# Optimization experiments

Measured on AMD Instinct MI355X. Metric: run time of the kernel, lower is better.

## Reference

```python
import jax, jax.numpy as jnp
import numpy as np

EPS = 1e-4
NEG_BIAS = 0.01


def setup_inputs() -> dict:
    key = jax.random.key(0)
    ks = jax.random.split(key, 9)
    B, L, D_MODEL, HALF = 4, 4096, 2048, 32
    return {
        "u": jax.random.normal(ks[0], (B, L, D_MODEL), dtype=jnp.float32),
        "Lambda_unconstrained_re": jax.random.normal(ks[1], (HALF,), dtype=jnp.float32) * 0.1 - 1.0,
        "Lambda_im": jax.random.normal(ks[2], (HALF,), dtype=jnp.float32) * 3.0,
        "B_re": jax.random.normal(ks[3], (HALF, D_MODEL), dtype=jnp.float32) * 0.02,
        "B_im": jax.random.normal(ks[4], (HALF, D_MODEL), dtype=jnp.float32) * 0.02,
        "C_re": jax.random.normal(ks[5], (D_MODEL, HALF), dtype=jnp.float32) * 0.05,
        "C_im": jax.random.normal(ks[6], (D_MODEL, HALF), dtype=jnp.float32) * 0.05,
        "D": jax.random.normal(ks[7], (D_MODEL,), dtype=jnp.float32) * 0.1,
        "log_Delta": jax.random.uniform(ks[8], (2 * HALF,), minval=-3.0, maxval=-1.0, dtype=jnp.float32),
    }


def reference(u, Lambda_unconstrained_re, Lambda_im, B_re, B_im, C_re, C_im, D, log_Delta):
    half = Lambda_im.shape[0]
    # Constrained continuous-time eigenvalues: Re < 0 via softplus (inverse of init formula)
    lam_re = -(jax.nn.softplus(Lambda_unconstrained_re) + EPS + NEG_BIAS)
    Lam = lam_re + 1j * Lambda_im                      # [half]
    Delta = jnp.exp(log_Delta[:half])                  # per-state timestep
    # ZOH discretization
    Lam_bar = jnp.exp(Lam * Delta)                     # [half]
    B_tilde = (B_re + 1j * B_im).astype(jnp.complex64) # [half, d]
    B_bar = ((Lam_bar - 1.0) / Lam)[:, None] * B_tilde # [half, d]
    # Input projection: Bu[b,l,n]
    Bu = jnp.einsum("bld,nd->bln", u.astype(jnp.complex64), B_bar)
    a = jnp.broadcast_to(Lam_bar, Bu.shape)

    def op(e1, e2):
        a1, b1 = e1
        a2, b2 = e2
        return (a1 * a2, a2 * b1 + b2)

    # Parallel associative scan of x_t = Lam_bar * x_{t-1} + Bu_t along time axis
    _, xs = jax.lax.associative_scan(op, (a, Bu), axis=1)  # [b, l, half]
    C_tilde = (C_re + 1j * C_im).astype(jnp.complex64)     # [d, half]
    # Conjugate symmetry -> 2 * real part, plus skip connection D * u
    y = 2.0 * jnp.real(jnp.einsum("bln,dn->bld", xs, C_tilde)) + D * u
    return y
```

## Files before the change

kernel.cpp:

```cpp
#include <hip/hip_runtime.h>
#include <math.h>

#define M_ROWS 16384
#define DM     2048
#define NJ     64
#define L_SEQ  4096

typedef __bf16 bf16x8 __attribute__((ext_vector_type(8)));
typedef float  f32x4  __attribute__((ext_vector_type(4)));

constexpr size_t OB_BBART = 0;
constexpr size_t OB_CCT   = 256 * 1024;
constexpr size_t OB_BUT   = 512 * 1024;
constexpr size_t OB_XST   = 512 * 1024 + 4194304;

static __device__ __forceinline__ unsigned short f2bf(float f) {
  unsigned int u = __float_as_uint(f);
  u = (u + 0x7fffu + ((u >> 16) & 1u)) >> 16;
  return (unsigned short)u;
}

__global__ void k_prep(const float* __restrict__ lam_ur, const float* __restrict__ lam_im,
                       const float* __restrict__ log_dt,
                       const float* __restrict__ Bre, const float* __restrict__ Bim,
                       const float* __restrict__ Cre, const float* __restrict__ Cim,
                       unsigned short* __restrict__ bbarT, unsigned short* __restrict__ ccT) {
  const int idx = blockIdx.x * 256 + threadIdx.x;
  {
    const int j = idx >> 11, d = idx & 2047, n = j >> 1;
    float x = lam_ur[n];
    float sp = (x > 20.f) ? x : log1pf(expf(x));
    float lre = -(sp + 1.0e-4f + 0.01f);
    float lim = lam_im[n];
    float dt = expf(log_dt[n]);
    float er = expf(lre * dt);
    float Are = er * cosf(lim * dt);
    float Aim = er * sinf(lim * dt);
    float den = lre * lre + lim * lim;
    float cre = ((Are - 1.f) * lre + Aim * lim) / den;
    float cim = (Aim * lre - (Are - 1.f) * lim) / den;
    float br = Bre[n * DM + d], bi = Bim[n * DM + d];
    float v = (j & 1) ? (cre * bi + cim * br) : (cre * br - cim * bi);
    bbarT[(size_t)j * DM + d] = f2bf(v);
  }
  {
    const int j = idx & 63, d = idx >> 6, n = j >> 1;
    float v = (j & 1) ? (-2.f * Cim[d * 32 + n]) : (2.f * Cre[d * 32 + n]);
    ccT[(size_t)d * NJ + j] = f2bf(v);
  }
}

__global__ __launch_bounds__(256) void k_bu(const float* __restrict__ u,
                                            const unsigned short* __restrict__ bbarT,
                                            float* __restrict__ bu_t) {
  __shared__ __align__(16) unsigned short As[16][72];
  const int t = threadIdx.x;
  const int wave = t >> 6, lane = t & 63;
  const int m0 = blockIdx.x * 16;
  const int l15 = lane & 15, kq8 = (lane >> 4) * 8;
  const int srow = t >> 4, scol = (t & 15) * 4;
  const float* up = u + (size_t)(m0 + srow) * DM + scol;
  const unsigned short* bp = bbarT + (size_t)(wave * 16 + l15) * DM + kq8;
  f32x4 acc = {0.f, 0.f, 0.f, 0.f};
  for (int k0 = 0; k0 < DM; k0 += 64) {
    float4 v = *(const float4*)(up + k0);
    __syncthreads();
    ushort4 w4;
    w4.x = f2bf(v.x); w4.y = f2bf(v.y); w4.z = f2bf(v.z); w4.w = f2bf(v.w);
    *(ushort4*)&As[srow][scol] = w4;
    __syncthreads();
    bf16x8 a0 = *(const bf16x8*)&As[l15][kq8];
    bf16x8 a1 = *(const bf16x8*)&As[l15][32 + kq8];
    bf16x8 b0 = *(const bf16x8*)(bp + k0);
    bf16x8 b1 = *(const bf16x8*)(bp + k0 + 32);
    acc = __builtin_amdgcn_mfma_f32_16x16x32_bf16(a0, b0, acc, 0, 0, 0);
    acc = __builtin_amdgcn_mfma_f32_16x16x32_bf16(a1, b1, acc, 0, 0, 0);
  }
  const int j = wave * 16 + l15;
  const int orow = m0 + (lane >> 4) * 4;
  *(f32x4*)&bu_t[(size_t)j * M_ROWS + orow] = acc;
}

__global__ __launch_bounds__(256) void k_scan(const float* __restrict__ bu_t,
                                              const float* __restrict__ lam_ur,
                                              const float* __restrict__ lam_im,
                                              const float* __restrict__ log_dt,
                                              unsigned short* __restrict__ xs_t) {
  __shared__ float sre[L_SEQ + 256], sim[L_SEQ + 256];
  __shared__ float2 P[256];
  const int n = blockIdx.x;
  const int b = blockIdx.y;
  const int t = threadIdx.x;
  float x = lam_ur[n];
  float sp = (x > 20.f) ? x : log1pf(expf(x));
  float lre = -(sp + 1.0e-4f + 0.01f);
  float lim = lam_im[n];
  float dt = expf(log_dt[n]);
  float er = expf(lre * dt);
  const float Are = er * cosf(lim * dt);
  const float Aim = er * sinf(lim * dt);
  const float* pr = bu_t + (size_t)(2 * n) * M_ROWS + (size_t)b * L_SEQ;
  const float* pi = bu_t + (size_t)(2 * n + 1) * M_ROWS + (size_t)b * L_SEQ;
#pragma unroll
  for (int i0 = 4 * t; i0 < L_SEQ; i0 += 1024) {
    float4 vr = *(const float4*)(pr + i0);
    float4 vi = *(const float4*)(pi + i0);
    const float rr[4] = {vr.x, vr.y, vr.z, vr.w};
    const float ii[4] = {vi.x, vi.y, vi.z, vi.w};
#pragma unroll
    for (int q = 0; q < 4; ++q) {
      int e = i0 + q, ee = e + (e >> 4);
      sre[ee] = rr[q];
      sim[ee] = ii[q];
    }
  }
  __syncthreads();
  float lre16[16], lim16[16];
  float xre = 0.f, xim = 0.f;
#pragma unroll
  for (int i = 0; i < 16; ++i) {
    float bre = sre[17 * t + i], bim = sim[17 * t + i];
    float nr = Are * xre - Aim * xim + bre;
    float ni = Are * xim + Aim * xre + bim;
    xre = nr; xim = ni;
    lre16[i] = nr; lim16[i] = ni;
  }
  float Mre = Are, Mim = Aim;
#pragma unroll
  for (int k = 0; k < 4; ++k) {
    float nr = Mre * Mre - Mim * Mim;
    float ni = 2.f * Mre * Mim;
    Mre = nr; Mim = ni;
  }
  float pre = xre, pim = xim;
  P[t] = make_float2(pre, pim);
  __syncthreads();
  float msre = Mre, msim = Mim;
  for (int s = 1; s < 256; s <<= 1) {
    float2 prev = (t >= s) ? P[t - s] : make_float2(0.f, 0.f);
    __syncthreads();
    pre += msre * prev.x - msim * prev.y;
    pim += msre * prev.y + msim * prev.x;
    P[t] = make_float2(pre, pim);
    float nr = msre * msre - msim * msim;
    float ni = 2.f * msre * msim;
    msre = nr; msim = ni;
    __syncthreads();
  }
  float2 E = (t == 0) ? make_float2(0.f, 0.f) : P[t - 1];
  float pwre = Are, pwim = Aim;
#pragma unroll
  for (int i = 0; i < 16; ++i) {
    sre[17 * t + i] = lre16[i] + pwre * E.x - pwim * E.y;
    sim[17 * t + i] = lim16[i] + pwre * E.y + pwim * E.x;
    float nr = pwre * Are - pwim * Aim;
    float ni = pwre * Aim + pwim * Are;
    pwre = nr; pwim = ni;
  }
  __syncthreads();
  unsigned int* xr = (unsigned int*)(xs_t + (size_t)(2 * n) * M_ROWS + (size_t)b * L_SEQ);
  unsigned int* xi = (unsigned int*)(xs_t + (size_t)(2 * n + 1) * M_ROWS + (size_t)b * L_SEQ);
  for (int i = t; i < L_SEQ / 2; i += 256) {
    int e0 = 2 * i, e1 = 2 * i + 1;
    int p0 = e0 + (e0 >> 4), p1 = e1 + (e1 >> 4);
    xr[i] = ((unsigned int)f2bf(sre[p1]) << 16) | f2bf(sre[p0]);
    xi[i] = ((unsigned int)f2bf(sim[p1]) << 16) | f2bf(sim[p0]);
  }
}

__global__ __launch_bounds__(256) void k_out(const unsigned short* __restrict__ xs_t,
                                             const unsigned short* __restrict__ ccT,
                                             const float* __restrict__ u,
                                             const float* __restrict__ Dv,
                                             float* __restrict__ y) {
  __shared__ __align__(16) char smem[64 * 132 * 4];
  unsigned short (*As)[72] = (unsigned short(*)[72])smem;
  float (*Es)[132] = (float(*)[132])smem;
  const int t = threadIdx.x;
  const int wave = t >> 6, lane = t & 63;
  const int m0 = blockIdx.x * 64;
  const int d0 = blockIdx.y * 128;
  const int l15 = lane & 15, kq8 = (lane >> 4) * 8;
#pragma unroll
  for (int p = 0; p < 8; ++p) {
    int idx = t + 256 * p;
    int j = idx >> 5, r2 = idx & 31;
    unsigned int v = *(const unsigned int*)(xs_t + (size_t)j * M_ROWS + m0 + 2 * r2);
    As[2 * r2][j] = (unsigned short)(v & 0xffffu);
    As[2 * r2 + 1][j] = (unsigned short)(v >> 16);
  }
  __syncthreads();
  bf16x8 a0 = *(const bf16x8*)&As[wave * 16 + l15][kq8];
  bf16x8 a1 = *(const bf16x8*)&As[wave * 16 + l15][32 + kq8];
  f32x4 acc[8];
#pragma unroll
  for (int c = 0; c < 8; ++c) acc[c] = (f32x4){0.f, 0.f, 0.f, 0.f};
#pragma unroll
  for (int c = 0; c < 8; ++c) {
    const unsigned short* cp = ccT + (size_t)(d0 + c * 16 + l15) * NJ + kq8;
    bf16x8 b0 = *(const bf16x8*)cp;
    bf16x8 b1 = *(const bf16x8*)(cp + 32);
    acc[c] = __builtin_amdgcn_mfma_f32_16x16x32_bf16(a0, b0, acc[c], 0, 0, 0);
    acc[c] = __builtin_amdgcn_mfma_f32_16x16x32_bf16(a1, b1, acc[c], 0, 0, 0);
  }
  __syncthreads();
#pragma unroll
  for (int c = 0; c < 8; ++c)
#pragma unroll
    for (int i = 0; i < 4; ++i)
      Es[wave * 16 + (lane >> 4) * 4 + i][c * 16 + l15] = acc[c][i];
  __syncthreads();
#pragma unroll
  for (int p = 0; p < 8; ++p) {
    int idx = t + 256 * p;
    int row = idx >> 5;
    int c4 = (idx & 31) * 4;
    f32x4 e = *(const f32x4*)&Es[row][c4];
    const size_t off = (size_t)(m0 + row) * DM + d0 + c4;
    float4 uu = *(const float4*)&u[off];
    float4 dd = *(const float4*)&Dv[d0 + c4];
    float4 o;
    o.x = e[0] + dd.x * uu.x;
    o.y = e[1] + dd.y * uu.y;
    o.z = e[2] + dd.z * uu.z;
    o.w = e[3] + dd.w * uu.w;
    *(float4*)&y[off] = o;
  }
}

extern "C" void kernel_launch(void* const* d_in, const int* in_sizes, int n_in,
                              void* d_out, int out_size, void* d_ws, size_t ws_size,
                              hipStream_t stream) {
  const float* u      = (const float*)d_in[0];
  const float* lam_ur = (const float*)d_in[1];
  const float* lam_im = (const float*)d_in[2];
  const float* B_re   = (const float*)d_in[3];
  const float* B_im   = (const float*)d_in[4];
  const float* C_re   = (const float*)d_in[5];
  const float* C_im   = (const float*)d_in[6];
  const float* Dv     = (const float*)d_in[7];
  const float* log_dt = (const float*)d_in[8];
  float* y = (float*)d_out;
  char* ws = (char*)d_ws;

  unsigned short* bbarT = (unsigned short*)(ws + OB_BBART);
  unsigned short* ccT   = (unsigned short*)(ws + OB_CCT);
  float*          bu_t  = (float*)(ws + OB_BUT);
  unsigned short* xs_t  = (unsigned short*)(ws + OB_XST);

  k_prep<<<512, 256, 0, stream>>>(lam_ur, lam_im, log_dt, B_re, B_im, C_re, C_im, bbarT, ccT);
  k_bu<<<M_ROWS / 16, 256, 0, stream>>>(u, bbarT, bu_t);
  k_scan<<<dim3(32, 4), 256, 0, stream>>>(bu_t, lam_ur, lam_im, log_dt, xs_t);
  k_out<<<dim3(M_ROWS / 64, DM / 128), 256, 0, stream>>>(xs_t, ccT, u, Dv, y);
}
```

Before: 299.8 us.

## Load GEMM operands directly into MFMA registers and make xs row-major

k_bu now loads u straight from global memory in the MFMA A-fragment layout and converts it to bf16 in registers. This removes the LDS staging and the two barriers per k-step, at the cost of each wave re-reading the same u rows. The scan output xs is switched from a transposed [j][m] layout to row-major [m][64], with real and imaginary parts packed into one word. k_out can then load its A fragments directly with vector loads instead of going through an LDS transpose and a barrier. The scan's stores become strided by 128 bytes, so they are no longer coalesced.

```diff
diff --git a/kernel.cpp b/kernel.cpp
--- a/kernel.cpp
+++ b/kernel.cpp
@@ -18,6 +18,15 @@
   unsigned int u = __float_as_uint(f);
   u = (u + 0x7fffu + ((u >> 16) & 1u)) >> 16;
   return (unsigned short)u;
+}
+
+union BF8 { unsigned short s[8]; bf16x8 v; };
+
+static __device__ __forceinline__ bf16x8 cvt8(float4 a, float4 b) {
+  BF8 r;
+  r.s[0] = f2bf(a.x); r.s[1] = f2bf(a.y); r.s[2] = f2bf(a.z); r.s[3] = f2bf(a.w);
+  r.s[4] = f2bf(b.x); r.s[5] = f2bf(b.y); r.s[6] = f2bf(b.z); r.s[7] = f2bf(b.w);
+  return r.v;
 }
 
 __global__ void k_prep(const float* __restrict__ lam_ur, const float* __restrict__ lam_im,
@@ -53,28 +62,19 @@
 __global__ __launch_bounds__(256) void k_bu(const float* __restrict__ u,
                                             const unsigned short* __restrict__ bbarT,
                                             float* __restrict__ bu_t) {
-  __shared__ __align__(16) unsigned short As[16][72];
   const int t = threadIdx.x;
   const int wave = t >> 6, lane = t & 63;
   const int m0 = blockIdx.x * 16;
   const int l15 = lane & 15, kq8 = (lane >> 4) * 8;
-  const int srow = t >> 4, scol = (t & 15) * 4;
-  const float* up = u + (size_t)(m0 + srow) * DM + scol;
+  const float* up = u + (size_t)(m0 + l15) * DM + kq8;
   const unsigned short* bp = bbarT + (size_t)(wave * 16 + l15) * DM + kq8;
   f32x4 acc = {0.f, 0.f, 0.f, 0.f};
-  for (int k0 = 0; k0 < DM; k0 += 64) {
-    float4 v = *(const float4*)(up + k0);
-    __syncthreads();
-    ushort4 w4;
-    w4.x = f2bf(v.x); w4.y = f2bf(v.y); w4.z = f2bf(v.z); w4.w = f2bf(v.w);
-    *(ushort4*)&As[srow][scol] = w4;
-    __syncthreads();
-    bf16x8 a0 = *(const bf16x8*)&As[l15][kq8];
-    bf16x8 a1 = *(const bf16x8*)&As[l15][32 + kq8];
-    bf16x8 b0 = *(const bf16x8*)(bp + k0);
-    bf16x8 b1 = *(const bf16x8*)(bp + k0 + 32);
-    acc = __builtin_amdgcn_mfma_f32_16x16x32_bf16(a0, b0, acc, 0, 0, 0);
-    acc = __builtin_amdgcn_mfma_f32_16x16x32_bf16(a1, b1, acc, 0, 0, 0);
+#pragma unroll 4
+  for (int k0 = 0; k0 < DM; k0 += 32) {
+    float4 v0 = *(const float4*)(up + k0);
+    float4 v1 = *(const float4*)(up + k0 + 4);
+    bf16x8 b = *(const bf16x8*)(bp + k0);
+    acc = __builtin_amdgcn_mfma_f32_16x16x32_bf16(cvt8(v0, v1), b, acc, 0, 0, 0);
   }
   const int j = wave * 16 + l15;
   const int orow = m0 + (lane >> 4) * 4;
@@ -158,13 +158,10 @@
     pwre = nr; pwim = ni;
   }
   __syncthreads();
-  unsigned int* xr = (unsigned int*)(xs_t + (size_t)(2 * n) * M_ROWS + (size_t)b * L_SEQ);
-  unsigned int* xi = (unsigned int*)(xs_t + (size_t)(2 * n + 1) * M_ROWS + (size_t)b * L_SEQ);
-  for (int i = t; i < L_SEQ / 2; i += 256) {
-    int e0 = 2 * i, e1 = 2 * i + 1;
-    int p0 = e0 + (e0 >> 4), p1 = e1 + (e1 >> 4);
-    xr[i] = ((unsigned int)f2bf(sre[p1]) << 16) | f2bf(sre[p0]);
-    xi[i] = ((unsigned int)f2bf(sim[p1]) << 16) | f2bf(sim[p0]);
+  unsigned int* xp = (unsigned int*)(xs_t + (size_t)b * L_SEQ * NJ + 2 * n);
+  for (int i = t; i < L_SEQ; i += 256) {
+    int p = i + (i >> 4);
+    xp[(size_t)i * (NJ / 2)] = ((unsigned int)f2bf(sim[p]) << 16) | f2bf(sre[p]);
   }
 }
 
@@ -173,25 +170,15 @@
                                              const float* __restrict__ u,
                                              const float* __restrict__ Dv,
                                              float* __restrict__ y) {
-  __shared__ __align__(16) char smem[64 * 132 * 4];
-  unsigned short (*As)[72] = (unsigned short(*)[72])smem;
-  float (*Es)[132] = (float(*)[132])smem;
+  __shared__ __align__(16) float Es[64][132];
   const int t = threadIdx.x;
   const int wave = t >> 6, lane = t & 63;
   const int m0 = blockIdx.x * 64;
   const int d0 = blockIdx.y * 128;
   const int l15 = lane & 15, kq8 = (lane >> 4) * 8;
-#pragma unroll
-  for (int p = 0; p < 8; ++p) {
-    int idx = t + 256 * p;
-    int j = idx >> 5, r2 = idx & 31;
-    unsigned int v = *(const unsigned int*)(xs_t + (size_t)j * M_ROWS + m0 + 2 * r2);
-    As[2 * r2][j] = (unsigned short)(v & 0xffffu);
-    As[2 * r2 + 1][j] = (unsigned short)(v >> 16);
-  }
-  __syncthreads();
-  bf16x8 a0 = *(const bf16x8*)&As[wave * 16 + l15][kq8];
-  bf16x8 a1 = *(const bf16x8*)&As[wave * 16 + l15][32 + kq8];
+  const unsigned short* ap = xs_t + (size_t)(m0 + wave * 16 + l15) * NJ;
+  bf16x8 a0 = *(const bf16x8*)(ap + kq8);
+  bf16x8 a1 = *(const bf16x8*)(ap + 32 + kq8);
   f32x4 acc[8];
 #pragma unroll
   for (int c = 0; c < 8; ++c) acc[c] = (f32x4){0.f, 0.f, 0.f, 0.f};
@@ -203,7 +190,6 @@
     acc[c] = __builtin_amdgcn_mfma_f32_16x16x32_bf16(a0, b0, acc[c], 0, 0, 0);
     acc[c] = __builtin_amdgcn_mfma_f32_16x16x32_bf16(a1, b1, acc[c], 0, 0, 0);
   }
-  __syncthreads();
 #pragma unroll
   for (int c = 0; c < 8; ++c)
 #pragma unroll
```

Result: slower. 335.1 us (+11.8%).
